# Kernel optimization log

Measured on AMD Instinct MI355X. Metric: run time of the kernel, lower is better.

## Reference

```python
import jax, jax.numpy as jnp
import numpy as np

B = 16384
F = 128   # num_features
H = 128   # hidden_dim
E = 32    # embedding_dim


def setup_inputs() -> dict:
    key = jax.random.key(0)
    k_x, k_w1, k_b1, k_w2, k_b2 = jax.random.split(key, 5)
    # Per-feature params stacked along feature axis.
    # Layer 1: Linear(1 -> H): weight [F, H] (in_dim==1 squeezed), bias [F, H]
    # Layer 2: Linear(H -> E): weight [F, H, E], bias [F, E]
    # Torch default init: U(-1/sqrt(fan_in), 1/sqrt(fan_in))
    w1 = jax.random.uniform(k_w1, (F, H), jnp.float32, -1.0, 1.0)          # fan_in=1
    b1 = jax.random.uniform(k_b1, (F, H), jnp.float32, -1.0, 1.0)
    bound2 = 1.0 / np.sqrt(H)
    w2 = jax.random.uniform(k_w2, (F, H, E), jnp.float32, -bound2, bound2)
    b2 = jax.random.uniform(k_b2, (F, E), jnp.float32, -bound2, bound2)
    x = jax.random.normal(k_x, (B, F), jnp.float32)
    return {"x": x, "w1": w1, "b1": b1, "w2": w2, "b2": b2}


def reference(x, w1, b1, w2, b2):
    # Fused over features: broadcast-mul replaces K=1 matmuls,
    # single batched GEMM replaces per-feature second Linear.
    h = jax.nn.relu(x[:, :, None] * w1[None] + b1[None])   # [B, F, H]
    out = jnp.einsum('bfh,fhe->bfe', h, w2) + b2[None]      # [B, F, E]
    return out.reshape(x.shape[0], F * E)                   # concat along last dim
```

## Files before the change

kernel.cpp:

```cpp
#include <hip/hip_runtime.h>
#include <math.h>

#define B_N 16384
#define F_N 128
#define H_N 128
#define E_N 32
#define ROWS (H_N + 1)

__global__ __launch_bounds__(128) void build_tables(
    const float* __restrict__ w1, const float* __restrict__ b1,
    const float* __restrict__ w2, const float* __restrict__ b2,
    float* __restrict__ ts_out, float* __restrict__ tab)
{
    __shared__ float w1s[H_N], b1s[H_N], ts[H_N];
    __shared__ int   hidx[H_N];
    __shared__ float w2s[H_N * E_N];
    __shared__ float dA[H_N * E_N];
    __shared__ float dC[H_N * E_N];
    __shared__ float baseA[4 * E_N], baseC[4 * E_N];

    const int f   = blockIdx.x;
    const int tid = threadIdx.x;

    float w1v = w1[f * H_N + tid];
    float b1v = b1[f * H_N + tid];
    w1s[tid] = w1v;
    b1s[tid] = b1v;
    ts[tid]   = (w1v != 0.0f) ? (-b1v / w1v) : INFINITY;
    hidx[tid] = tid;

    {
        const float4* src = (const float4*)(w2 + (size_t)f * H_N * E_N);
        float4*       dst = (float4*)w2s;
        #pragma unroll
        for (int it = 0; it < 8; ++it) dst[it * 128 + tid] = src[it * 128 + tid];
    }
    __syncthreads();

    for (int k = 2; k <= H_N; k <<= 1) {
        for (int j = k >> 1; j > 0; j >>= 1) {
            int ixj = tid ^ j;
            if (ixj > tid) {
                float a = ts[tid], bv = ts[ixj];
                bool up = ((tid & k) == 0);
                bool sw = up ? (a > bv) : (a < bv);
                if (sw) {
                    int ia = hidx[tid];
                    ts[tid] = bv; ts[ixj] = a;
                    hidx[tid] = hidx[ixj]; hidx[ixj] = ia;
                }
            }
            __syncthreads();
        }
    }

    ts_out[f * H_N + tid] = ts[tid];

    const int e = tid & 31;
    const int g = tid >> 5;

    #pragma unroll 4
    for (int jj = 0; jj < 32; ++jj) {
        int   j   = g * 32 + jj;
        int   p   = hidx[j];
        float w1h = w1s[p], b1h = b1s[p];
        float w2v = w2s[p * E_N + e];
        float s   = (w1h > 0.f) ? 1.f : ((w1h < 0.f) ? -1.f : 0.f);
        dA[j * E_N + e] = s * w1h * w2v;
        dC[j * E_N + e] = s * b1h * w2v;
    }
    {
        float pA = 0.f, pC = 0.f;
        #pragma unroll 4
        for (int hh = 0; hh < 32; ++hh) {
            int   h   = g * 32 + hh;
            float w1h = w1s[h], b1h = b1s[h];
            float w2v = w2s[h * E_N + e];
            if (w1h < 0.f) {
                pA = fmaf(w1h, w2v, pA);
                pC = fmaf(b1h, w2v, pC);
            } else if (w1h == 0.f && b1h > 0.f) {
                pC = fmaf(b1h, w2v, pC);
            }
        }
        baseA[g * E_N + e] = pA;
        baseC[g * E_N + e] = pC;
    }
    __syncthreads();

    if (tid < E_N) {
        float accA = baseA[e] + baseA[E_N + e] + baseA[2 * E_N + e] + baseA[3 * E_N + e];
        float accC = baseC[e] + baseC[E_N + e] + baseC[2 * E_N + e] + baseC[3 * E_N + e];
        accC += b2[f * E_N + e];
        const size_t base = (size_t)f * ROWS * 64;
        tab[base + e]        = accA;
        tab[base + 32 + e]   = accC;
        for (int j = 0; j < H_N; ++j) {
            accA += dA[j * E_N + e];
            accC += dC[j * E_N + e];
            tab[base + (size_t)(j + 1) * 64 + e]      = accA;
            tab[base + (size_t)(j + 1) * 64 + 32 + e] = accC;
        }
    }
}

#define FH 32
#define NB 64
#define CH 8

__global__ __launch_bounds__(256) void apply_tables(
    const float* __restrict__ x, const float* __restrict__ ts,
    const float* __restrict__ tab, float* __restrict__ out)
{
    __shared__ float lds_t[FH * ROWS];
    __shared__ float xs[NB * FH];

    const int tid = threadIdx.x;
    const int b0  = blockIdx.x * NB;
    const int f0  = blockIdx.y * FH;

    {
        const float4* src = (const float4*)(ts + (size_t)f0 * H_N);
        #pragma unroll
        for (int it = 0; it < (FH * H_N / 4) / 256; ++it) {
            int    vi  = it * 256 + tid;
            float4 v   = src[vi];
            int    idx = vi * 4;
            int    fl  = idx >> 7;
            int    j   = idx & 127;
            float* dst = &lds_t[fl * ROWS + j];
            dst[0] = v.x; dst[1] = v.y; dst[2] = v.z; dst[3] = v.w;
        }
    }
    {
        #pragma unroll
        for (int it = 0; it < (NB * FH / 4) / 256; ++it) {
            int vi = it * 256 + tid;
            int bl = vi >> 3;
            int fq = (vi & 7) * 4;
            float4 v = *(const float4*)(x + (size_t)(b0 + bl) * F_N + f0 + fq);
            *(float4*)(&xs[bl * FH + fq]) = v;
        }
    }
    __syncthreads();

    const int fl = tid >> 3;
    const int eq = tid & 7;
    const int fg = f0 + fl;
    const float* tloc     = &lds_t[fl * ROWS];
    const size_t tab_base = (size_t)fg * ROWS * 64 + eq * 4;
    const size_t out_base = (size_t)b0 * (F_N * E_N) + (size_t)fg * E_N + eq * 4;

    for (int c = 0; c < NB / CH; ++c) {
        float xv[CH];
        int   lo[CH], hi[CH];
        #pragma unroll
        for (int j = 0; j < CH; ++j) {
            xv[j] = xs[(c * CH + j) * FH + fl];
            lo[j] = 0;
            hi[j] = H_N;
        }
        #pragma unroll
        for (int s = 0; s < 7; ++s) {
            #pragma unroll
            for (int j = 0; j < CH; ++j) {
                int  mid = (lo[j] + hi[j]) >> 1;
                bool lt  = tloc[mid] < xv[j];
                lo[j] = lt ? mid + 1 : lo[j];
                hi[j] = lt ? hi[j] : mid;
            }
        }
        #pragma unroll
        for (int j = 0; j < CH; ++j) {
            const float* row = tab + tab_base + (size_t)lo[j] * 64;
            float4 a4 = *(const float4*)(row);
            float4 c4 = *(const float4*)(row + 32);
            float  xj = xv[j];
            float4 o;
            o.x = fmaf(xj, a4.x, c4.x);
            o.y = fmaf(xj, a4.y, c4.y);
            o.z = fmaf(xj, a4.z, c4.z);
            o.w = fmaf(xj, a4.w, c4.w);
            *(float4*)(out + out_base + (size_t)(c * CH + j) * (F_N * E_N)) = o;
        }
    }
}

__global__ __launch_bounds__(256) void direct_kernel(
    const float* __restrict__ x, const float* __restrict__ w1,
    const float* __restrict__ b1, const float* __restrict__ w2,
    const float* __restrict__ b2, float* __restrict__ out)
{
    __shared__ float w1s[H_N], b1s[H_N], b2s[E_N];
    __shared__ float w2s[H_N * E_N];
    const int f   = blockIdx.y;
    const int tid = threadIdx.x;
    if (tid < H_N) { w1s[tid] = w1[f * H_N + tid]; b1s[tid] = b1[f * H_N + tid]; }
    for (int i = tid; i < H_N * E_N; i += 256) w2s[i] = w2[(size_t)f * H_N * E_N + i];
    if (tid < E_N) b2s[tid] = b2[f * E_N + tid];
    __syncthreads();

    const int b  = blockIdx.x * 256 + tid;
    float xv = x[(size_t)b * F_N + f];
    float acc[E_N];
    #pragma unroll
    for (int e = 0; e < E_N; ++e) acc[e] = b2s[e];
    for (int h = 0; h < H_N; ++h) {
        float hv = fmaxf(fmaf(xv, w1s[h], b1s[h]), 0.f);
        #pragma unroll
        for (int e = 0; e < E_N; ++e) acc[e] = fmaf(hv, w2s[h * E_N + e], acc[e]);
    }
    float* op = out + (size_t)b * (F_N * E_N) + (size_t)f * E_N;
    #pragma unroll
    for (int e = 0; e < E_N; e += 4)
        *(float4*)(op + e) = make_float4(acc[e], acc[e + 1], acc[e + 2], acc[e + 3]);
}

extern "C" void kernel_launch(void* const* d_in, const int* in_sizes, int n_in,
                              void* d_out, int out_size, void* d_ws, size_t ws_size,
                              hipStream_t stream) {
    const float* x  = (const float*)d_in[0];
    const float* w1 = (const float*)d_in[1];
    const float* b1 = (const float*)d_in[2];
    const float* w2 = (const float*)d_in[3];
    const float* b2 = (const float*)d_in[4];
    float* out = (float*)d_out;

    const size_t n_ts  = (size_t)F_N * H_N;
    const size_t n_tab = (size_t)F_N * ROWS * 64;
    const size_t need  = (n_ts + n_tab) * sizeof(float);

    if (ws_size >= need) {
        float* ts  = (float*)d_ws;
        float* tab = ts + n_ts;
        build_tables<<<dim3(F_N), dim3(128), 0, stream>>>(w1, b1, w2, b2, ts, tab);
        apply_tables<<<dim3(B_N / NB, F_N / FH), dim3(256), 0, stream>>>(x, ts, tab, out);
    } else {
        direct_kernel<<<dim3(B_N / 256, F_N), dim3(256), 0, stream>>>(x, w1, b1, w2, b2, out);
    }
}
```

Baseline: 334.1 us.

## Deduplicate binary search via LDS index table and interleave A/C table rows

Each (batch, feature) segment index is now computed once per block into a shared ushort table. Before, all 8 threads sharing a feature repeated the same 7-step binary search. The precomputed table rows are interleaved so each thread's A and C float4s sit next to each other in one 32-byte span, and the batch tile is halved to 32 to raise block count. Gathers are batched before the FMAs to expose more memory-level parallelism. The cost is an extra sync and a bit more LDS.

```diff
diff --git a/kernel.cpp b/kernel.cpp
--- a/kernel.cpp
+++ b/kernel.cpp
@@ -93,27 +93,29 @@
         float accC = baseC[e] + baseC[E_N + e] + baseC[2 * E_N + e] + baseC[3 * E_N + e];
         accC += b2[f * E_N + e];
         const size_t base = (size_t)f * ROWS * 64;
-        tab[base + e]        = accA;
-        tab[base + 32 + e]   = accC;
+        const int    off  = ((e >> 2) * 8) + (e & 3);
+        tab[base + off]     = accA;
+        tab[base + off + 4] = accC;
         for (int j = 0; j < H_N; ++j) {
             accA += dA[j * E_N + e];
             accC += dC[j * E_N + e];
-            tab[base + (size_t)(j + 1) * 64 + e]      = accA;
-            tab[base + (size_t)(j + 1) * 64 + 32 + e] = accC;
+            tab[base + (size_t)(j + 1) * 64 + off]     = accA;
+            tab[base + (size_t)(j + 1) * 64 + off + 4] = accC;
         }
     }
 }
 
 #define FH 32
-#define NB 64
+#define NB 32
 #define CH 8
 
 __global__ __launch_bounds__(256) void apply_tables(
     const float* __restrict__ x, const float* __restrict__ ts,
     const float* __restrict__ tab, float* __restrict__ out)
 {
-    __shared__ float lds_t[FH * ROWS];
-    __shared__ float xs[NB * FH];
+    __shared__ float          lds_t[FH * ROWS];
+    __shared__ float          xs[NB * FH];
+    __shared__ unsigned short ridx[NB * FH];
 
     const int tid = threadIdx.x;
     const int b0  = blockIdx.x * NB;
@@ -133,55 +135,75 @@
         }
     }
     {
-        #pragma unroll
-        for (int it = 0; it < (NB * FH / 4) / 256; ++it) {
-            int vi = it * 256 + tid;
-            int bl = vi >> 3;
-            int fq = (vi & 7) * 4;
-            float4 v = *(const float4*)(x + (size_t)(b0 + bl) * F_N + f0 + fq);
-            *(float4*)(&xs[bl * FH + fq]) = v;
-        }
+        int bl = tid >> 3;
+        int fq = (tid & 7) * 4;
+        float4 v = *(const float4*)(x + (size_t)(b0 + bl) * F_N + f0 + fq);
+        *(float4*)(&xs[bl * FH + fq]) = v;
+    }
+    __syncthreads();
+
+    {
+        int   lo[4], hi[4];
+        float xv[4];
+        const float* tl[4];
+        #pragma unroll
+        for (int k = 0; k < 4; ++k) {
+            int p  = k * 256 + tid;
+            int fl = p & (FH - 1);
+            int bl = p >> 5;
+            xv[k] = xs[bl * FH + fl];
+            tl[k] = &lds_t[fl * ROWS];
+            lo[k] = 0;
+            hi[k] = H_N;
+        }
+        #pragma unroll
+        for (int s = 0; s < 7; ++s) {
+            #pragma unroll
+            for (int k = 0; k < 4; ++k) {
+                int  mid = (lo[k] + hi[k]) >> 1;
+                bool lt  = tl[k][mid] < xv[k];
+                lo[k] = lt ? mid + 1 : lo[k];
+                hi[k] = lt ? hi[k] : mid;
+            }
+        }
+        #pragma unroll
+        for (int k = 0; k < 4; ++k)
+            ridx[k * 256 + tid] = (unsigned short)lo[k];
     }
     __syncthreads();
 
     const int fl = tid >> 3;
     const int eq = tid & 7;
     const int fg = f0 + fl;
-    const float* tloc     = &lds_t[fl * ROWS];
-    const size_t tab_base = (size_t)fg * ROWS * 64 + eq * 4;
-    const size_t out_base = (size_t)b0 * (F_N * E_N) + (size_t)fg * E_N + eq * 4;
-
+    const float* tabf     = tab + (size_t)fg * (ROWS * 64) + eq * 8;
+    float*       outp     = out + (size_t)b0 * (F_N * E_N) + (size_t)fg * E_N + eq * 4;
+
+    #pragma unroll 1
     for (int c = 0; c < NB / CH; ++c) {
+        int   r[CH];
         float xv[CH];
-        int   lo[CH], hi[CH];
         #pragma unroll
         for (int j = 0; j < CH; ++j) {
-            xv[j] = xs[(c * CH + j) * FH + fl];
-            lo[j] = 0;
-            hi[j] = H_N;
-        }
-        #pragma unroll
-        for (int s = 0; s < 7; ++s) {
-            #pragma unroll
-            for (int j = 0; j < CH; ++j) {
-                int  mid = (lo[j] + hi[j]) >> 1;
-                bool lt  = tloc[mid] < xv[j];
-                lo[j] = lt ? mid + 1 : lo[j];
-                hi[j] = lt ? hi[j] : mid;
-            }
-        }
+            int bl = c * CH + j;
+            r[j]  = ridx[bl * FH + fl];
+            xv[j] = xs[bl * FH + fl];
+        }
+        float4 a4[CH], c4[CH];
         #pragma unroll
         for (int j = 0; j < CH; ++j) {
-            const float* row = tab + tab_base + (size_t)lo[j] * 64;
-            float4 a4 = *(const float4*)(row);
-            float4 c4 = *(const float4*)(row + 32);
+            const float* row = tabf + (size_t)r[j] * 64;
+            a4[j] = *(const float4*)(row);
+            c4[j] = *(const float4*)(row + 4);
+        }
+        #pragma unroll
+        for (int j = 0; j < CH; ++j) {
             float  xj = xv[j];
             float4 o;
-            o.x = fmaf(xj, a4.x, c4.x);
-            o.y = fmaf(xj, a4.y, c4.y);
-            o.z = fmaf(xj, a4.z, c4.z);
-            o.w = fmaf(xj, a4.w, c4.w);
-            *(float4*)(out + out_base + (size_t)(c * CH + j) * (F_N * E_N)) = o;
+            o.x = fmaf(xj, a4[j].x, c4[j].x);
+            o.y = fmaf(xj, a4[j].y, c4[j].y);
+            o.z = fmaf(xj, a4[j].z, c4[j].z);
+            o.w = fmaf(xj, a4[j].w, c4[j].w);
+            *(float4*)(outp + (size_t)(c * CH + j) * (F_N * E_N)) = o;
         }
     }
 }
```

Measured after the change: 340.5 us. About the same (+1.9%).
